# Performance work log

Measured on AMD Instinct MI355X. Metric: run time of the kernel, lower is better.

## Reference

```python
import jax, jax.numpy as jnp
import numpy as np

H = 512   # embedding_dim (forced by Attention(512,512))
F = 21    # n_features
T = 28    # output_length

def _cell(x, h, c, Wih, Whh, b):
    # PyTorch LSTMCell math, gate order i,f,g,o
    g = x @ Wih.T + h @ Whh.T + b
    i, f, gg, o = jnp.split(g, 4, axis=-1)
    c2 = jax.nn.sigmoid(f) * c + jax.nn.sigmoid(i) * jnp.tanh(gg)
    h2 = jax.nn.sigmoid(o) * jnp.tanh(c2)
    return h2, c2

def _lstm3(inp, h, c, Wih0, Wih1, Wih2, Whh, bih, bhh):
    # 3-layer LSTM, single time step. h,c: [3,1,H]
    Wihs = (Wih0, Wih1, Wih2)
    hs, cs = [], []
    x = inp
    for l in range(3):
        hl, cl = _cell(x, h[l], c[l], Wihs[l], Whh[l], bih[l] + bhh[l])
        hs.append(hl); cs.append(cl)
        x = hl
    return x, jnp.stack(hs), jnp.stack(cs)

def setup_inputs() -> dict:
    key = jax.random.key(0)
    ks = jax.random.split(key, 20)
    s = 0.05
    f32 = jnp.float32
    return {
        "x": jax.random.normal(ks[0], (1, F), f32),
        "prev_y": jax.random.normal(ks[1], (1, F), f32),
        "enc_Wih0": jax.random.normal(ks[2], (4*H, F), f32) * s,
        "enc_Wih1": jax.random.normal(ks[3], (4*H, H), f32) * s,
        "enc_Wih2": jax.random.normal(ks[4], (4*H, H), f32) * s,
        "enc_Whh": jax.random.normal(ks[5], (3, 4*H, H), f32) * s,
        "enc_bih": jax.random.normal(ks[6], (3, 4*H), f32) * s,
        "enc_bhh": jax.random.normal(ks[7], (3, 4*H), f32) * s,
        "attn_W": jax.random.normal(ks[8], (H, 2*H), f32) * s,
        "attn_b": jax.random.normal(ks[9], (H,), f32) * s,
        "v_W": jax.random.normal(ks[10], (1, H), f32) * s,
        "dec_Wih0": jax.random.normal(ks[11], (4*H, H+F), f32) * s,
        "dec_Wih1": jax.random.normal(ks[12], (4*H, H), f32) * s,
        "dec_Wih2": jax.random.normal(ks[13], (4*H, H), f32) * s,
        "dec_Whh": jax.random.normal(ks[14], (3, 4*H, H), f32) * s,
        "dec_bih": jax.random.normal(ks[15], (3, 4*H), f32) * s,
        "dec_bhh": jax.random.normal(ks[16], (3, 4*H), f32) * s,
        "out_W": jax.random.normal(ks[17], (F, 2*H), f32) * s,
        "out_b": jax.random.normal(ks[18], (F,), f32) * s,
    }

def reference(x, prev_y, enc_Wih0, enc_Wih1, enc_Wih2, enc_Whh, enc_bih, enc_bhh,
              attn_W, attn_b, v_W, dec_Wih0, dec_Wih1, dec_Wih2, dec_Whh, dec_bih, dec_bhh,
              out_W, out_b):
    z = jnp.zeros((3, 1, H), x.dtype)
    # Encoder: single time step over feature-as-sequence input [1, F]
    enc_out, h, c = _lstm3(x, z, z, enc_Wih0, enc_Wih1, enc_Wih2, enc_Whh, enc_bih, enc_bhh)
    # enc_out: [1, H]; src_len == 1

    def step(carry, _):
        prev_out, h, c = carry
        # Bahdanau attention (src_len = 1)
        cat = jnp.concatenate([h[2], enc_out], axis=-1)          # [1, 2H]
        energy = jnp.tanh(cat @ attn_W.T + attn_b)               # [1, H]
        score = energy @ v_W.T                                    # [1, 1]
        a = jax.nn.softmax(score, axis=1)                         # [1, 1] (== 1)
        weighted = a * enc_out                                    # [1, H]
        rnn_in = jnp.concatenate([prev_out, weighted], axis=-1)  # [1, H+F]
        out, h2, c2 = _lstm3(rnn_in, h, c, dec_Wih0, dec_Wih1, dec_Wih2, dec_Whh, dec_bih, dec_bhh)
        y = jnp.concatenate([out, weighted], axis=-1) @ out_W.T + out_b  # [1, F]
        return (y, h2, c2), y

    _, ys = jax.lax.scan(step, (prev_y, h, c), None, length=T)
    return ys  # [T, 1, F]
```

## Files before the change

### kernel.cpp

```cpp
#include <hip/hip_runtime.h>
#include <cstddef>

constexpr int H  = 512;
constexpr int F  = 21;
constexpr int T  = 28;
constexpr int NB = 128;
constexpr int NT = 256;
constexpr int NW = NT / 64;

#define SCOPE_AGENT __HIP_MEMORY_SCOPE_AGENT

__device__ unsigned long long g_hp[2][3][H];
__device__ unsigned g_exit;

struct P {
  const float *x, *py, *eW0, *eW1, *eW2, *ebih, *ebhh;
  const float *dW0, *dW1, *dW2, *dWhh, *dbih, *dbhh, *outW, *outb;
  float* out;
};

__device__ __forceinline__ float sigm(float v)  { return 1.0f / (1.0f + __expf(-v)); }
__device__ __forceinline__ float tanh_f(float v){ return 1.0f - 2.0f / (__expf(2.0f * v) + 1.0f); }

__device__ __forceinline__ float4 wredsum4(float4 v) {
#pragma unroll
  for (int off = 32; off > 0; off >>= 1) {
    v.x += __shfl_xor(v.x, off, 64);
    v.y += __shfl_xor(v.y, off, 64);
    v.z += __shfl_xor(v.z, off, 64);
    v.w += __shfl_xor(v.w, off, 64);
  }
  return v;
}
__device__ __forceinline__ float wredsum1(float v) {
#pragma unroll
  for (int off = 32; off > 0; off >>= 1) v += __shfl_xor(v, off, 64);
  return v;
}

__device__ __forceinline__ void pput(unsigned long long* slot, float v, unsigned tag) {
  union { float f; unsigned u; } c; c.f = v;
  unsigned long long pk = ((unsigned long long)tag << 32) | (unsigned long long)c.u;
  (void)__hip_atomic_exchange(slot, pk, __ATOMIC_RELAXED, SCOPE_AGENT);
}
__device__ __forceinline__ unsigned long long tld(const unsigned long long* q) {
  return __hip_atomic_load(q, __ATOMIC_RELAXED, SCOPE_AGENT);
}
__device__ __forceinline__ float fbits(unsigned long long v) {
  union { unsigned u; float f; } c; c.u = (unsigned)v; return c.f;
}

__device__ __forceinline__ void stagev(const unsigned long long* __restrict__ A,
                                       unsigned wa, float* __restrict__ dst) {
  const int i = threadIdx.x;
  unsigned long long v0 = tld(A + i), v1 = tld(A + i + NT);
  int guard = 0;
  while ((((unsigned)(v0 >> 32)) != wa || ((unsigned)(v1 >> 32)) != wa) &&
         ++guard < (1 << 20)) {
    v0 = tld(A + i); v1 = tld(A + i + NT);
  }
  dst[i] = fbits(v0); dst[i + NT] = fbits(v1);
  __syncthreads();
}

__device__ __forceinline__ void pollvec8(const unsigned long long* __restrict__ A,
                                         int lane, unsigned want, float4& x0, float4& x1) {
  const unsigned long long* q = A + lane * 8;
  unsigned long long v[8];
#pragma unroll
  for (int k = 0; k < 8; ++k) v[k] = tld(q + k);
  int guard = 0;
  for (;;) {
    bool ok = true;
#pragma unroll
    for (int k = 0; k < 8; ++k) ok &= ((unsigned)(v[k] >> 32) == want);
    if (ok || ++guard > (1 << 20)) break;
#pragma unroll
    for (int k = 0; k < 8; ++k) v[k] = tld(q + k);
  }
  x0 = make_float4(fbits(v[0]), fbits(v[1]), fbits(v[2]), fbits(v[3]));
  x1 = make_float4(fbits(v[4]), fbits(v[5]), fbits(v[6]), fbits(v[7]));
}

struct W8 { float4 a[4]; float4 b[4]; };

__device__ __forceinline__ W8 ldw_g(const float* __restrict__ W, int r, int lane) {
  W8 o;
#pragma unroll
  for (int g = 0; g < 4; ++g) {
    const float* q = W + (size_t)(g * H + r) * H + lane * 8;
    o.a[g] = *(const float4*)q;
    o.b[g] = *(const float4*)(q + 4);
  }
  return o;
}
__device__ __forceinline__ W8 ldw_lds(const float* sM, int w, int lane) {
  W8 o;
#pragma unroll
  for (int g = 0; g < 4; ++g) {
    const float* q = sM + (w * 4 + g) * H + lane * 8;
    o.a[g] = *(const float4*)q;
    o.b[g] = *(const float4*)(q + 4);
  }
  return o;
}
__device__ __forceinline__ void fma8(const W8& wt, const float4& x0, const float4& x1,
                                     float s[4]) {
#pragma unroll
  for (int g = 0; g < 4; ++g) {
    s[g] += wt.a[g].x * x0.x + wt.a[g].y * x0.y + wt.a[g].z * x0.z + wt.a[g].w * x0.w
          + wt.b[g].x * x1.x + wt.b[g].y * x1.y + wt.b[g].z * x1.z + wt.b[g].w * x1.w;
  }
}

__device__ __forceinline__ float cellup(const float4& v, const float b[4], float& c) {
  float cn = sigm(v.y + b[1]) * c + sigm(v.x + b[0]) * tanh_f(v.z + b[2]);
  c = cn;
  return sigm(v.w + b[3]) * tanh_f(cn);
}

__device__ __forceinline__ void write_y(const P& p, int trow, int w, int lane,
                                        const float4& h0, const float4& h1,
                                        const float* sYe) {
  for (int j = w; j < F; j += NW) {
    const float* q = p.outW + (size_t)j * (2 * H) + lane * 8;
    float4 w0 = *(const float4*)q;
    float4 w1 = *(const float4*)(q + 4);
    float s = w0.x * h0.x + w0.y * h0.y + w0.z * h0.z + w0.w * h0.w
            + w1.x * h1.x + w1.y * h1.y + w1.z * h1.z + w1.w * h1.w;
    s = wredsum1(s);
    if (lane == 0) p.out[trow * F + j] = s + sYe[j];
  }
}

__global__ __launch_bounds__(NT, 1)
void k_flow(P p) {
  const int lane = threadIdx.x & 63;
  const int w    = threadIdx.x >> 6;
  const int r    = blockIdx.x * NW + w;

  __shared__ float sM[NW * 4 * H];
  __shared__ float sBuf[2][H];
  __shared__ float senc[H];
  __shared__ float sYe[F + 3];
  __shared__ int   s_last;

  float c0 = 0.f, c1 = 0.f, c2 = 0.f;
  float b00[4], b0p[4], b1s[4], b2s[4];
  float sOld0[4] = {0, 0, 0, 0}, sOld1[4] = {0, 0, 0, 0}, sOld2[4] = {0, 0, 0, 0};
  int bi = 0;

  {
    float s0 = 0.f, s1 = 0.f, s2 = 0.f, s3 = 0.f;
    if (lane < F) {
      const float xv = p.x[lane];
      s0 = p.eW0[(size_t)(0 * H + r) * F + lane] * xv;
      s1 = p.eW0[(size_t)(1 * H + r) * F + lane] * xv;
      s2 = p.eW0[(size_t)(2 * H + r) * F + lane] * xv;
      s3 = p.eW0[(size_t)(3 * H + r) * F + lane] * xv;
    }
    float4 v = wredsum4(make_float4(s0, s1, s2, s3));
    if (lane == 0) {
      const float* bi_ = p.ebih + r;
      const float* bh_ = p.ebhh + r;
      float cn = sigm(v.x + bi_[0] + bh_[0]) * tanh_f(v.z + bi_[2 * H] + bh_[2 * H]);
      c0 = cn;
      pput(&g_hp[1][0][r], sigm(v.w + bi_[3 * H] + bh_[3 * H]) * tanh_f(cn), 1u);
    }
  }

  {
    float4 mA[4], mB[4];
#pragma unroll
    for (int g = 0; g < 4; ++g) {
      mA[g] = make_float4(0.f, 0.f, 0.f, 0.f);
      mB[g] = make_float4(0.f, 0.f, 0.f, 0.f);
    }
    for (int f = 0; f < F; ++f) {
      const float* q = p.outW + (size_t)f * (2 * H) + lane * 8;
      const float4 oa = *(const float4*)q;
      const float4 ob = *(const float4*)(q + 4);
#pragma unroll
      for (int g = 0; g < 4; ++g) {
        const float wf = p.dW0[(size_t)(g * H + r) * (H + F) + f];
        mA[g].x += wf * oa.x; mA[g].y += wf * oa.y; mA[g].z += wf * oa.z; mA[g].w += wf * oa.w;
        mB[g].x += wf * ob.x; mB[g].y += wf * ob.y; mB[g].z += wf * ob.z; mB[g].w += wf * ob.w;
      }
    }
#pragma unroll
    for (int g = 0; g < 4; ++g) {
      *(float4*)(sM + (w * 4 + g) * H + lane * 8)     = mA[g];
      *(float4*)(sM + (w * 4 + g) * H + lane * 8 + 4) = mB[g];
    }
  }
#pragma unroll
  for (int g = 0; g < 4; ++g) {
    b1s[g] = p.dbih[4 * H + g * H + r] + p.dbhh[4 * H + g * H + r];
    b2s[g] = p.dbih[8 * H + g * H + r] + p.dbhh[8 * H + g * H + r];
  }

  {
    W8 wt = ldw_g(p.eW1, r, lane);
    stagev(g_hp[1][0], 1u, sBuf[0]);
    float4 a0 = *(const float4*)(sBuf[0] + lane * 8);
    float4 a1 = *(const float4*)(sBuf[0] + lane * 8 + 4);
    float s[4] = {0.f, 0.f, 0.f, 0.f};
    fma8(wt, a0, a1, s);
    float4 v = wredsum4(make_float4(s[0], s[1], s[2], s[3]));
    if (lane == 0) {
      const float* bi_ = p.ebih + 4 * H + r;
      const float* bh_ = p.ebhh + 4 * H + r;
      float cn = sigm(v.x + bi_[0] + bh_[0]) * tanh_f(v.z + bi_[2 * H] + bh_[2 * H]);
      c1 = cn;
      pput(&g_hp[1][1][r], sigm(v.w + bi_[3 * H] + bh_[3 * H]) * tanh_f(cn), 1u);
    }
  }

  {
    W8 wt  = ldw_g(p.eW2, r, lane);
    W8 wh1 = ldw_g(p.dWhh + (size_t)4 * H * H, r, lane);
    stagev(g_hp[1][1], 1u, sBuf[1]);
    float4 a0 = *(const float4*)(sBuf[1] + lane * 8);
    float4 a1 = *(const float4*)(sBuf[1] + lane * 8 + 4);
    float s[4] = {0.f, 0.f, 0.f, 0.f};
    fma8(wt, a0, a1, s);
    float4 v = wredsum4(make_float4(s[0], s[1], s[2], s[3]));
    if (lane == 0) {
      const float* bi_ = p.ebih + 8 * H + r;
      const float* bh_ = p.ebhh + 8 * H + r;
      float cn = sigm(v.x + bi_[0] + bh_[0]) * tanh_f(v.z + bi_[2 * H] + bh_[2 * H]);
      c2 = cn;
      pput(&g_hp[1][2][r], sigm(v.w + bi_[3 * H] + bh_[3 * H]) * tanh_f(cn), 1u);
    }
    fma8(wh1, a0, a1, sOld1);
  }

  {
    W8 wh2 = ldw_g(p.dWhh + (size_t)8 * H * H, r, lane);
    stagev(g_hp[1][2], 1u, senc);
    float4 e0 = *(const float4*)(senc + lane * 8);
    float4 e1 = *(const float4*)(senc + lane * 8 + 4);
    for (int j = w; j < F; j += NW) {
      const float* q = p.outW + (size_t)j * (2 * H) + H + lane * 8;
      float4 w0 = *(const float4*)q;
      float4 w1 = *(const float4*)(q + 4);
      float s = w0.x * e0.x + w0.y * e0.y + w0.z * e0.z + w0.w * e0.w
              + w1.x * e1.x + w1.y * e1.y + w1.z * e1.z + w1.w * e1.w;
      s = wredsum1(s);
      if (lane == 0) sYe[j] = s + p.outb[j];
    }
    {
      float sg[4];
#pragma unroll
      for (int g = 0; g < 4; ++g) {
        const float* q = p.dW0 + (size_t)(g * H + r) * (H + F) + F + lane * 8;
        sg[g] = q[0] * e0.x + q[1] * e0.y + q[2] * e0.z + q[3] * e0.w
              + q[4] * e1.x + q[5] * e1.y + q[6] * e1.z + q[7] * e1.w;
      }
      float4 v = wredsum4(make_float4(sg[0], sg[1], sg[2], sg[3]));
      if (lane == 0) {
        b0p[0] = v.x + p.dbih[0 * H + r] + p.dbhh[0 * H + r];
        b0p[1] = v.y + p.dbih[1 * H + r] + p.dbhh[1 * H + r];
        b0p[2] = v.z + p.dbih[2 * H + r] + p.dbhh[2 * H + r];
        b0p[3] = v.w + p.dbih[3 * H + r] + p.dbhh[3 * H + r];
      }
    }
    {
      float f0 = 0.f, f1 = 0.f, f2 = 0.f, f3 = 0.f;
      if (lane < F) {
        const float yv = p.py[lane];
        f0 = p.dW0[(size_t)(0 * H + r) * (H + F) + lane] * yv;
        f1 = p.dW0[(size_t)(1 * H + r) * (H + F) + lane] * yv;
        f2 = p.dW0[(size_t)(2 * H + r) * (H + F) + lane] * yv;
        f3 = p.dW0[(size_t)(3 * H + r) * (H + F) + lane] * yv;
      }
      float4 v = wredsum4(make_float4(f0, f1, f2, f3));
      if (lane == 0) {
        b00[0] = b0p[0] + v.x; b00[1] = b0p[1] + v.y;
        b00[2] = b0p[2] + v.z; b00[3] = b0p[3] + v.w;
      }
    }
    __syncthreads();
    {
      float f0 = 0.f, f1 = 0.f, f2 = 0.f, f3 = 0.f;
      if (lane < F) {
        const float yv = sYe[lane];
        f0 = p.dW0[(size_t)(0 * H + r) * (H + F) + lane] * yv;
        f1 = p.dW0[(size_t)(1 * H + r) * (H + F) + lane] * yv;
        f2 = p.dW0[(size_t)(2 * H + r) * (H + F) + lane] * yv;
        f3 = p.dW0[(size_t)(3 * H + r) * (H + F) + lane] * yv;
      }
      float4 v = wredsum4(make_float4(f0, f1, f2, f3));
      if (lane == 0) {
        b0p[0] += v.x; b0p[1] += v.y; b0p[2] += v.z; b0p[3] += v.w;
      }
    }
    fma8(wh2, e0, e1, sOld2);
  }

  {
    W8 wh0 = ldw_g(p.dWhh, r, lane);
    float4 a0 = *(const float4*)(sBuf[0] + lane * 8);
    float4 a1 = *(const float4*)(sBuf[0] + lane * 8 + 4);
    float s[4] = {0.f, 0.f, 0.f, 0.f};
    fma8(wh0, a0, a1, s);
    float4 v = wredsum4(make_float4(s[0], s[1], s[2], s[3]));
    if (lane == 0) pput(&g_hp[0][0][r], cellup(v, b00, c0), 2u);
  }
  __syncthreads();

  for (int t = 0; t < T; ++t) {
    const int pb = t & 1, ob = pb ^ 1;
    const unsigned wn = (unsigned)(t + 2);
    const unsigned wo = (unsigned)(t + 1);

    if (t >= 1) {
      W8 wh2 = ldw_g(p.dWhh + (size_t)8 * H * H, r, lane);
      stagev(g_hp[ob][2], wo, sBuf[bi]);
      W8 wm = ldw_lds(sM, w, lane);
      float4 h20 = *(const float4*)(sBuf[bi] + lane * 8);
      float4 h21 = *(const float4*)(sBuf[bi] + lane * 8 + 4);
      float s[4] = {sOld0[0], sOld0[1], sOld0[2], sOld0[3]};
      fma8(wm, h20, h21, s);
      float4 v = wredsum4(make_float4(s[0], s[1], s[2], s[3]));
      if (lane == 0) pput(&g_hp[pb][0][r], cellup(v, b0p, c0), wn);
      if (blockIdx.x == (unsigned)t) write_y(p, t - 1, w, lane, h20, h21, sYe);
      sOld2[0] = sOld2[1] = sOld2[2] = sOld2[3] = 0.f;
      fma8(wh2, h20, h21, sOld2);
      bi ^= 1;
    }

    {
      W8 wi  = ldw_g(p.dW1, r, lane);
      W8 wh0 = ldw_g(p.dWhh, r, lane);
      stagev(g_hp[pb][0], wn, sBuf[bi]);
      float4 a0 = *(const float4*)(sBuf[bi] + lane * 8);
      float4 a1 = *(const float4*)(sBuf[bi] + lane * 8 + 4);
      float s[4] = {sOld1[0], sOld1[1], sOld1[2], sOld1[3]};
      fma8(wi, a0, a1, s);
      float4 v = wredsum4(make_float4(s[0], s[1], s[2], s[3]));
      if (lane == 0) pput(&g_hp[pb][1][r], cellup(v, b1s, c1), wn);
      sOld0[0] = sOld0[1] = sOld0[2] = sOld0[3] = 0.f;
      fma8(wh0, a0, a1, sOld0);
      bi ^= 1;
    }
    {
      W8 wi  = ldw_g(p.dW2, r, lane);
      W8 wh1 = ldw_g(p.dWhh + (size_t)4 * H * H, r, lane);
      stagev(g_hp[pb][1], wn, sBuf[bi]);
      float4 a0 = *(const float4*)(sBuf[bi] + lane * 8);
      float4 a1 = *(const float4*)(sBuf[bi] + lane * 8 + 4);
      float s[4] = {sOld2[0], sOld2[1], sOld2[2], sOld2[3]};
      fma8(wi, a0, a1, s);
      float4 v = wredsum4(make_float4(s[0], s[1], s[2], s[3]));
      if (lane == 0) pput(&g_hp[pb][2][r], cellup(v, b2s, c2), wn);
      sOld1[0] = sOld1[1] = sOld1[2] = sOld1[3] = 0.f;
      fma8(wh1, a0, a1, sOld1);
      bi ^= 1;
    }
  }

  if (blockIdx.x == (unsigned)T) {
    float4 h20, h21;
    pollvec8(g_hp[(T - 1) & 1][2], lane, (unsigned)(T + 1), h20, h21);
    write_y(p, T - 1, w, lane, h20, h21, sYe);
  }

  __syncthreads();
  if (threadIdx.x == 0) {
    unsigned old = __hip_atomic_fetch_add(&g_exit, 1u, __ATOMIC_RELAXED, SCOPE_AGENT);
    s_last = (old == NB - 1) ? 1 : 0;
  }
  __syncthreads();
  if (s_last) {
    unsigned long long* z = &g_hp[0][0][0];
    for (int i = threadIdx.x; i < 2 * 3 * H; i += NT)
      __hip_atomic_store(z + i, 0ull, __ATOMIC_RELAXED, SCOPE_AGENT);
    if (threadIdx.x == 0)
      __hip_atomic_store(&g_exit, 0u, __ATOMIC_RELAXED, SCOPE_AGENT);
  }
}

extern "C" void kernel_launch(void* const* d_in, const int* in_sizes, int n_in,
                              void* d_out, int out_size, void* d_ws, size_t ws_size,
                              hipStream_t stream) {
  P p;
  p.x    = (const float*)d_in[0];
  p.py   = (const float*)d_in[1];
  p.eW0  = (const float*)d_in[2];
  p.eW1  = (const float*)d_in[3];
  p.eW2  = (const float*)d_in[4];
  p.ebih = (const float*)d_in[6];
  p.ebhh = (const float*)d_in[7];
  p.dW0  = (const float*)d_in[11];
  p.dW1  = (const float*)d_in[12];
  p.dW2  = (const float*)d_in[13];
  p.dWhh = (const float*)d_in[14];
  p.dbih = (const float*)d_in[15];
  p.dbhh = (const float*)d_in[16];
  p.outW = (const float*)d_in[17];
  p.outb = (const float*)d_in[18];
  p.out  = (float*)d_out;

  hipLaunchKernelGGL(k_flow, dim3(NB), dim3(NT), 0, stream, p);
}
```

Measured before the change: 356.5 us.

## Move output projection to a dedicated extra block fed by per-step h buffers

Adds a 129th block that only computes the per-step output projection y, reading each step's top-layer hidden state from a new per-timestep global buffer g_hy. The recurrent blocks no longer run write_y on their critical path, and the final-step polling block is removed. In exchange, each step's top-layer store doubles, another block is launched, and there are more global buffers to clear at exit.

```diff
diff --git a/kernel.cpp b/kernel.cpp
--- a/kernel.cpp
+++ b/kernel.cpp
@@ -4,13 +4,15 @@
 constexpr int H  = 512;
 constexpr int F  = 21;
 constexpr int T  = 28;
-constexpr int NB = 128;
+constexpr int PB = 128;
+constexpr int NB = PB + 1;
 constexpr int NT = 256;
 constexpr int NW = NT / 64;
 
 #define SCOPE_AGENT __HIP_MEMORY_SCOPE_AGENT
 
 __device__ unsigned long long g_hp[2][3][H];
+__device__ unsigned long long g_hy[T][H];
 __device__ unsigned g_exit;
 
 struct P {
@@ -63,25 +65,6 @@
   __syncthreads();
 }
 
-__device__ __forceinline__ void pollvec8(const unsigned long long* __restrict__ A,
-                                         int lane, unsigned want, float4& x0, float4& x1) {
-  const unsigned long long* q = A + lane * 8;
-  unsigned long long v[8];
-#pragma unroll
-  for (int k = 0; k < 8; ++k) v[k] = tld(q + k);
-  int guard = 0;
-  for (;;) {
-    bool ok = true;
-#pragma unroll
-    for (int k = 0; k < 8; ++k) ok &= ((unsigned)(v[k] >> 32) == want);
-    if (ok || ++guard > (1 << 20)) break;
-#pragma unroll
-    for (int k = 0; k < 8; ++k) v[k] = tld(q + k);
-  }
-  x0 = make_float4(fbits(v[0]), fbits(v[1]), fbits(v[2]), fbits(v[3]));
-  x1 = make_float4(fbits(v[4]), fbits(v[5]), fbits(v[6]), fbits(v[7]));
-}
-
 struct W8 { float4 a[4]; float4 b[4]; };
 
 __device__ __forceinline__ W8 ldw_g(const float* __restrict__ W, int r, int lane) {
@@ -119,9 +102,9 @@
   return sigm(v.w + b[3]) * tanh_f(cn);
 }
 
-__device__ __forceinline__ void write_y(const P& p, int trow, int w, int lane,
-                                        const float4& h0, const float4& h1,
-                                        const float* sYe) {
+__device__ __forceinline__ void write_y_frag(const P& p, int trow, int w, int lane,
+                                             const float4& h0, const float4& h1,
+                                             const float* sYe) {
   for (int j = w; j < F; j += NW) {
     const float* q = p.outW + (size_t)j * (2 * H) + lane * 8;
     float4 w0 = *(const float4*)q;
@@ -137,7 +120,6 @@
 void k_flow(P p) {
   const int lane = threadIdx.x & 63;
   const int w    = threadIdx.x >> 6;
-  const int r    = blockIdx.x * NW + w;
 
   __shared__ float sM[NW * 4 * H];
   __shared__ float sBuf[2][H];
@@ -145,225 +127,249 @@
   __shared__ float sYe[F + 3];
   __shared__ int   s_last;
 
-  float c0 = 0.f, c1 = 0.f, c2 = 0.f;
-  float b00[4], b0p[4], b1s[4], b2s[4];
-  float sOld0[4] = {0, 0, 0, 0}, sOld1[4] = {0, 0, 0, 0}, sOld2[4] = {0, 0, 0, 0};
-  int bi = 0;
-
-  {
-    float s0 = 0.f, s1 = 0.f, s2 = 0.f, s3 = 0.f;
-    if (lane < F) {
-      const float xv = p.x[lane];
-      s0 = p.eW0[(size_t)(0 * H + r) * F + lane] * xv;
-      s1 = p.eW0[(size_t)(1 * H + r) * F + lane] * xv;
-      s2 = p.eW0[(size_t)(2 * H + r) * F + lane] * xv;
-      s3 = p.eW0[(size_t)(3 * H + r) * F + lane] * xv;
-    }
-    float4 v = wredsum4(make_float4(s0, s1, s2, s3));
-    if (lane == 0) {
-      const float* bi_ = p.ebih + r;
-      const float* bh_ = p.ebhh + r;
-      float cn = sigm(v.x + bi_[0] + bh_[0]) * tanh_f(v.z + bi_[2 * H] + bh_[2 * H]);
-      c0 = cn;
-      pput(&g_hp[1][0][r], sigm(v.w + bi_[3 * H] + bh_[3 * H]) * tanh_f(cn), 1u);
-    }
-  }
-
-  {
-    float4 mA[4], mB[4];
+  if (blockIdx.x == PB) {
+    stagev(g_hp[1][2], 1u, senc);
+    {
+      float4 e0 = *(const float4*)(senc + lane * 8);
+      float4 e1 = *(const float4*)(senc + lane * 8 + 4);
+      for (int j = w; j < F; j += NW) {
+        const float* q = p.outW + (size_t)j * (2 * H) + H + lane * 8;
+        float4 w0 = *(const float4*)q;
+        float4 w1 = *(const float4*)(q + 4);
+        float s = w0.x * e0.x + w0.y * e0.y + w0.z * e0.z + w0.w * e0.w
+                + w1.x * e1.x + w1.y * e1.y + w1.z * e1.z + w1.w * e1.w;
+        s = wredsum1(s);
+        if (lane == 0) sYe[j] = s + p.outb[j];
+      }
+      __syncthreads();
+    }
+    for (int t = 0; t < T; ++t) {
+      float* xb = sBuf[t & 1];
+      stagev(g_hy[t], (unsigned)(t + 2), xb);
+      float4 h20 = *(const float4*)(xb + lane * 8);
+      float4 h21 = *(const float4*)(xb + lane * 8 + 4);
+      write_y_frag(p, t, w, lane, h20, h21, sYe);
+    }
+  } else {
+    const int r = blockIdx.x * NW + w;
+
+    float c0 = 0.f, c1 = 0.f, c2 = 0.f;
+    float b00[4], b0p[4], b1s[4], b2s[4];
+    float sOld0[4] = {0, 0, 0, 0}, sOld1[4] = {0, 0, 0, 0}, sOld2[4] = {0, 0, 0, 0};
+    int bi = 0;
+
+    {
+      float s0 = 0.f, s1 = 0.f, s2 = 0.f, s3 = 0.f;
+      if (lane < F) {
+        const float xv = p.x[lane];
+        s0 = p.eW0[(size_t)(0 * H + r) * F + lane] * xv;
+        s1 = p.eW0[(size_t)(1 * H + r) * F + lane] * xv;
+        s2 = p.eW0[(size_t)(2 * H + r) * F + lane] * xv;
+        s3 = p.eW0[(size_t)(3 * H + r) * F + lane] * xv;
+      }
+      float4 v = wredsum4(make_float4(s0, s1, s2, s3));
+      if (lane == 0) {
+        const float* bi_ = p.ebih + r;
+        const float* bh_ = p.ebhh + r;
+        float cn = sigm(v.x + bi_[0] + bh_[0]) * tanh_f(v.z + bi_[2 * H] + bh_[2 * H]);
+        c0 = cn;
+        pput(&g_hp[1][0][r], sigm(v.w + bi_[3 * H] + bh_[3 * H]) * tanh_f(cn), 1u);
+      }
+    }
+
+    {
+      float4 mA[4], mB[4];
+#pragma unroll
+      for (int g = 0; g < 4; ++g) {
+        mA[g] = make_float4(0.f, 0.f, 0.f, 0.f);
+        mB[g] = make_float4(0.f, 0.f, 0.f, 0.f);
+      }
+      for (int f = 0; f < F; ++f) {
+        const float* q = p.outW + (size_t)f * (2 * H) + lane * 8;
+        const float4 oa = *(const float4*)q;
+        const float4 ob = *(const float4*)(q + 4);
+#pragma unroll
+        for (int g = 0; g < 4; ++g) {
+          const float wf = p.dW0[(size_t)(g * H + r) * (H + F) + f];
+          mA[g].x += wf * oa.x; mA[g].y += wf * oa.y; mA[g].z += wf * oa.z; mA[g].w += wf * oa.w;
+          mB[g].x += wf * ob.x; mB[g].y += wf * ob.y; mB[g].z += wf * ob.z; mB[g].w += wf * ob.w;
+        }
+      }
+#pragma unroll
+      for (int g = 0; g < 4; ++g) {
+        *(float4*)(sM + (w * 4 + g) * H + lane * 8)     = mA[g];
+        *(float4*)(sM + (w * 4 + g) * H + lane * 8 + 4) = mB[g];
+      }
+    }
 #pragma unroll
     for (int g = 0; g < 4; ++g) {
-      mA[g] = make_float4(0.f, 0.f, 0.f, 0.f);
-      mB[g] = make_float4(0.f, 0.f, 0.f, 0.f);
-    }
-    for (int f = 0; f < F; ++f) {
-      const float* q = p.outW + (size_t)f * (2 * H) + lane * 8;
-      const float4 oa = *(const float4*)q;
-      const float4 ob = *(const float4*)(q + 4);
-#pragma unroll
-      for (int g = 0; g < 4; ++g) {
-        const float wf = p.dW0[(size_t)(g * H + r) * (H + F) + f];
-        mA[g].x += wf * oa.x; mA[g].y += wf * oa.y; mA[g].z += wf * oa.z; mA[g].w += wf * oa.w;
-        mB[g].x += wf * ob.x; mB[g].y += wf * ob.y; mB[g].z += wf * ob.z; mB[g].w += wf * ob.w;
-      }
-    }
-#pragma unroll
-    for (int g = 0; g < 4; ++g) {
-      *(float4*)(sM + (w * 4 + g) * H + lane * 8)     = mA[g];
-      *(float4*)(sM + (w * 4 + g) * H + lane * 8 + 4) = mB[g];
-    }
-  }
-#pragma unroll
-  for (int g = 0; g < 4; ++g) {
-    b1s[g] = p.dbih[4 * H + g * H + r] + p.dbhh[4 * H + g * H + r];
-    b2s[g] = p.dbih[8 * H + g * H + r] + p.dbhh[8 * H + g * H + r];
-  }
-
-  {
-    W8 wt = ldw_g(p.eW1, r, lane);
-    stagev(g_hp[1][0], 1u, sBuf[0]);
-    float4 a0 = *(const float4*)(sBuf[0] + lane * 8);
-    float4 a1 = *(const float4*)(sBuf[0] + lane * 8 + 4);
-    float s[4] = {0.f, 0.f, 0.f, 0.f};
-    fma8(wt, a0, a1, s);
-    float4 v = wredsum4(make_float4(s[0], s[1], s[2], s[3]));
-    if (lane == 0) {
-      const float* bi_ = p.ebih + 4 * H + r;
-      const float* bh_ = p.ebhh + 4 * H + r;
-      float cn = sigm(v.x + bi_[0] + bh_[0]) * tanh_f(v.z + bi_[2 * H] + bh_[2 * H]);
-      c1 = cn;
-      pput(&g_hp[1][1][r], sigm(v.w + bi_[3 * H] + bh_[3 * H]) * tanh_f(cn), 1u);
-    }
-  }
-
-  {
-    W8 wt  = ldw_g(p.eW2, r, lane);
-    W8 wh1 = ldw_g(p.dWhh + (size_t)4 * H * H, r, lane);
-    stagev(g_hp[1][1], 1u, sBuf[1]);
-    float4 a0 = *(const float4*)(sBuf[1] + lane * 8);
-    float4 a1 = *(const float4*)(sBuf[1] + lane * 8 + 4);
-    float s[4] = {0.f, 0.f, 0.f, 0.f};
-    fma8(wt, a0, a1, s);
-    float4 v = wredsum4(make_float4(s[0], s[1], s[2], s[3]));
-    if (lane == 0) {
-      const float* bi_ = p.ebih + 8 * H + r;
-      const float* bh_ = p.ebhh + 8 * H + r;
-      float cn = sigm(v.x + bi_[0] + bh_[0]) * tanh_f(v.z + bi_[2 * H] + bh_[2 * H]);
-      c2 = cn;
-      pput(&g_hp[1][2][r], sigm(v.w + bi_[3 * H] + bh_[3 * H]) * tanh_f(cn), 1u);
-    }
-    fma8(wh1, a0, a1, sOld1);
-  }
-
-  {
-    W8 wh2 = ldw_g(p.dWhh + (size_t)8 * H * H, r, lane);
-    stagev(g_hp[1][2], 1u, senc);
-    float4 e0 = *(const float4*)(senc + lane * 8);
-    float4 e1 = *(const float4*)(senc + lane * 8 + 4);
-    for (int j = w; j < F; j += NW) {
-      const float* q = p.outW + (size_t)j * (2 * H) + H + lane * 8;
-      float4 w0 = *(const float4*)q;
-      float4 w1 = *(const float4*)(q + 4);
-      float s = w0.x * e0.x + w0.y * e0.y + w0.z * e0.z + w0.w * e0.w
-              + w1.x * e1.x + w1.y * e1.y + w1.z * e1.z + w1.w * e1.w;
-      s = wredsum1(s);
-      if (lane == 0) sYe[j] = s + p.outb[j];
-    }
-    {
-      float sg[4];
-#pragma unroll
-      for (int g = 0; g < 4; ++g) {
-        const float* q = p.dW0 + (size_t)(g * H + r) * (H + F) + F + lane * 8;
-        sg[g] = q[0] * e0.x + q[1] * e0.y + q[2] * e0.z + q[3] * e0.w
-              + q[4] * e1.x + q[5] * e1.y + q[6] * e1.z + q[7] * e1.w;
-      }
-      float4 v = wredsum4(make_float4(sg[0], sg[1], sg[2], sg[3]));
+      b1s[g] = p.dbih[4 * H + g * H + r] + p.dbhh[4 * H + g * H + r];
+      b2s[g] = p.dbih[8 * H + g * H + r] + p.dbhh[8 * H + g * H + r];
+    }
+
+    {
+      W8 wt = ldw_g(p.eW1, r, lane);
+      stagev(g_hp[1][0], 1u, sBuf[0]);
+      float4 a0 = *(const float4*)(sBuf[0] + lane * 8);
+      float4 a1 = *(const float4*)(sBuf[0] + lane * 8 + 4);
+      float s[4] = {0.f, 0.f, 0.f, 0.f};
+      fma8(wt, a0, a1, s);
+      float4 v = wredsum4(make_float4(s[0], s[1], s[2], s[3]));
       if (lane == 0) {
-        b0p[0] = v.x + p.dbih[0 * H + r] + p.dbhh[0 * H + r];
-        b0p[1] = v.y + p.dbih[1 * H + r] + p.dbhh[1 * H + r];
-        b0p[2] = v.z + p.dbih[2 * H + r] + p.dbhh[2 * H + r];
-        b0p[3] = v.w + p.dbih[3 * H + r] + p.dbhh[3 * H + r];
-      }
-    }
-    {
-      float f0 = 0.f, f1 = 0.f, f2 = 0.f, f3 = 0.f;
-      if (lane < F) {
-        const float yv = p.py[lane];
-        f0 = p.dW0[(size_t)(0 * H + r) * (H + F) + lane] * yv;
-        f1 = p.dW0[(size_t)(1 * H + r) * (H + F) + lane] * yv;
-        f2 = p.dW0[(size_t)(2 * H + r) * (H + F) + lane] * yv;
-        f3 = p.dW0[(size_t)(3 * H + r) * (H + F) + lane] * yv;
-      }
-      float4 v = wredsum4(make_float4(f0, f1, f2, f3));
+        const float* bi_ = p.ebih + 4 * H + r;
+        const float* bh_ = p.ebhh + 4 * H + r;
+        float cn = sigm(v.x + bi_[0] + bh_[0]) * tanh_f(v.z + bi_[2 * H] + bh_[2 * H]);
+        c1 = cn;
+        pput(&g_hp[1][1][r], sigm(v.w + bi_[3 * H] + bh_[3 * H]) * tanh_f(cn), 1u);
+      }
+    }
+
+    {
+      W8 wt  = ldw_g(p.eW2, r, lane);
+      W8 wh1 = ldw_g(p.dWhh + (size_t)4 * H * H, r, lane);
+      stagev(g_hp[1][1], 1u, sBuf[1]);
+      float4 a0 = *(const float4*)(sBuf[1] + lane * 8);
+      float4 a1 = *(const float4*)(sBuf[1] + lane * 8 + 4);
+      float s[4] = {0.f, 0.f, 0.f, 0.f};
+      fma8(wt, a0, a1, s);
+      float4 v = wredsum4(make_float4(s[0], s[1], s[2], s[3]));
       if (lane == 0) {
-        b00[0] = b0p[0] + v.x; b00[1] = b0p[1] + v.y;
-        b00[2] = b0p[2] + v.z; b00[3] = b0p[3] + v.w;
-      }
+        const float* bi_ = p.ebih + 8 * H + r;
+        const float* bh_ = p.ebhh + 8 * H + r;
+        float cn = sigm(v.x + bi_[0] + bh_[0]) * tanh_f(v.z + bi_[2 * H] + bh_[2 * H]);
+        c2 = cn;
+        pput(&g_hp[1][2][r], sigm(v.w + bi_[3 * H] + bh_[3 * H]) * tanh_f(cn), 1u);
+      }
+      fma8(wh1, a0, a1, sOld1);
+    }
+
+    {
+      W8 wh2 = ldw_g(p.dWhh + (size_t)8 * H * H, r, lane);
+      stagev(g_hp[1][2], 1u, senc);
+      float4 e0 = *(const float4*)(senc + lane * 8);
+      float4 e1 = *(const float4*)(senc + lane * 8 + 4);
+      for (int j = w; j < F; j += NW) {
+        const float* q = p.outW + (size_t)j * (2 * H) + H + lane * 8;
+        float4 w0 = *(const float4*)q;
+        float4 w1 = *(const float4*)(q + 4);
+        float s = w0.x * e0.x + w0.y * e0.y + w0.z * e0.z + w0.w * e0.w
+                + w1.x * e1.x + w1.y * e1.y + w1.z * e1.z + w1.w * e1.w;
+        s = wredsum1(s);
+        if (lane == 0) sYe[j] = s + p.outb[j];
+      }
+      {
+        float sg[4];
+#pragma unroll
+        for (int g = 0; g < 4; ++g) {
+          const float* q = p.dW0 + (size_t)(g * H + r) * (H + F) + F + lane * 8;
+          sg[g] = q[0] * e0.x + q[1] * e0.y + q[2] * e0.z + q[3] * e0.w
+                + q[4] * e1.x + q[5] * e1.y + q[6] * e1.z + q[7] * e1.w;
+        }
+        float4 v = wredsum4(make_float4(sg[0], sg[1], sg[2], sg[3]));
+        if (lane == 0) {
+          b0p[0] = v.x + p.dbih[0 * H + r] + p.dbhh[0 * H + r];
+          b0p[1] = v.y + p.dbih[1 * H + r] + p.dbhh[1 * H + r];
+          b0p[2] = v.z + p.dbih[2 * H + r] + p.dbhh[2 * H + r];
+          b0p[3] = v.w + p.dbih[3 * H + r] + p.dbhh[3 * H + r];
+        }
+      }
+      {
+        float f0 = 0.f, f1 = 0.f, f2 = 0.f, f3 = 0.f;
+        if (lane < F) {
+          const float yv = p.py[lane];
+          f0 = p.dW0[(size_t)(0 * H + r) * (H + F) + lane] * yv;
+          f1 = p.dW0[(size_t)(1 * H + r) * (H + F) + lane] * yv;
+          f2 = p.dW0[(size_t)(2 * H + r) * (H + F) + lane] * yv;
+          f3 = p.dW0[(size_t)(3 * H + r) * (H + F) + lane] * yv;
+        }
+        float4 v = wredsum4(make_float4(f0, f1, f2, f3));
+        if (lane == 0) {
+          b00[0] = b0p[0] + v.x; b00[1] = b0p[1] + v.y;
+          b00[2] = b0p[2] + v.z; b00[3] = b0p[3] + v.w;
+        }
+      }
+      __syncthreads();
+      {
+        float f0 = 0.f, f1 = 0.f, f2 = 0.f, f3 = 0.f;
+        if (lane < F) {
+          const float yv = sYe[lane];
+          f0 = p.dW0[(size_t)(0 * H + r) * (H + F) + lane] * yv;
+          f1 = p.dW0[(size_t)(1 * H + r) * (H + F) + lane] * yv;
+          f2 = p.dW0[(size_t)(2 * H + r) * (H + F) + lane] * yv;
+          f3 = p.dW0[(size_t)(3 * H + r) * (H + F) + lane] * yv;
+        }
+        float4 v = wredsum4(make_float4(f0, f1, f2, f3));
+        if (lane == 0) {
+          b0p[0] += v.x; b0p[1] += v.y; b0p[2] += v.z; b0p[3] += v.w;
+        }
+      }
+      fma8(wh2, e0, e1, sOld2);
+    }
+
+    {
+      W8 wh0 = ldw_g(p.dWhh, r, lane);
+      float4 a0 = *(const float4*)(sBuf[0] + lane * 8);
+      float4 a1 = *(const float4*)(sBuf[0] + lane * 8 + 4);
+      float s[4] = {0.f, 0.f, 0.f, 0.f};
+      fma8(wh0, a0, a1, s);
+      float4 v = wredsum4(make_float4(s[0], s[1], s[2], s[3]));
+      if (lane == 0) pput(&g_hp[0][0][r], cellup(v, b00, c0), 2u);
     }
     __syncthreads();
-    {
-      float f0 = 0.f, f1 = 0.f, f2 = 0.f, f3 = 0.f;
-      if (lane < F) {
-        const float yv = sYe[lane];
-        f0 = p.dW0[(size_t)(0 * H + r) * (H + F) + lane] * yv;
-        f1 = p.dW0[(size_t)(1 * H + r) * (H + F) + lane] * yv;
-        f2 = p.dW0[(size_t)(2 * H + r) * (H + F) + lane] * yv;
-        f3 = p.dW0[(size_t)(3 * H + r) * (H + F) + lane] * yv;
-      }
-      float4 v = wredsum4(make_float4(f0, f1, f2, f3));
-      if (lane == 0) {
-        b0p[0] += v.x; b0p[1] += v.y; b0p[2] += v.z; b0p[3] += v.w;
-      }
-    }
-    fma8(wh2, e0, e1, sOld2);
-  }
-
-  {
-    W8 wh0 = ldw_g(p.dWhh, r, lane);
-    float4 a0 = *(const float4*)(sBuf[0] + lane * 8);
-    float4 a1 = *(const float4*)(sBuf[0] + lane * 8 + 4);
-    float s[4] = {0.f, 0.f, 0.f, 0.f};
-    fma8(wh0, a0, a1, s);
-    float4 v = wredsum4(make_float4(s[0], s[1], s[2], s[3]));
-    if (lane == 0) pput(&g_hp[0][0][r], cellup(v, b00, c0), 2u);
-  }
-  __syncthreads();
-
-  for (int t = 0; t < T; ++t) {
-    const int pb = t & 1, ob = pb ^ 1;
-    const unsigned wn = (unsigned)(t + 2);
-    const unsigned wo = (unsigned)(t + 1);
-
-    if (t >= 1) {
-      W8 wh2 = ldw_g(p.dWhh + (size_t)8 * H * H, r, lane);
-      stagev(g_hp[ob][2], wo, sBuf[bi]);
-      W8 wm = ldw_lds(sM, w, lane);
-      float4 h20 = *(const float4*)(sBuf[bi] + lane * 8);
-      float4 h21 = *(const float4*)(sBuf[bi] + lane * 8 + 4);
-      float s[4] = {sOld0[0], sOld0[1], sOld0[2], sOld0[3]};
-      fma8(wm, h20, h21, s);
-      float4 v = wredsum4(make_float4(s[0], s[1], s[2], s[3]));
-      if (lane == 0) pput(&g_hp[pb][0][r], cellup(v, b0p, c0), wn);
-      if (blockIdx.x == (unsigned)t) write_y(p, t - 1, w, lane, h20, h21, sYe);
-      sOld2[0] = sOld2[1] = sOld2[2] = sOld2[3] = 0.f;
-      fma8(wh2, h20, h21, sOld2);
-      bi ^= 1;
-    }
-
-    {
-      W8 wi  = ldw_g(p.dW1, r, lane);
-      W8 wh0 = ldw_g(p.dWhh, r, lane);
-      stagev(g_hp[pb][0], wn, sBuf[bi]);
-      float4 a0 = *(const float4*)(sBuf[bi] + lane * 8);
-      float4 a1 = *(const float4*)(sBuf[bi] + lane * 8 + 4);
-      float s[4] = {sOld1[0], sOld1[1], sOld1[2], sOld1[3]};
-      fma8(wi, a0, a1, s);
-      float4 v = wredsum4(make_float4(s[0], s[1], s[2], s[3]));
-      if (lane == 0) pput(&g_hp[pb][1][r], cellup(v, b1s, c1), wn);
-      sOld0[0] = sOld0[1] = sOld0[2] = sOld0[3] = 0.f;
-      fma8(wh0, a0, a1, sOld0);
-      bi ^= 1;
-    }
-    {
-      W8 wi  = ldw_g(p.dW2, r, lane);
-      W8 wh1 = ldw_g(p.dWhh + (size_t)4 * H * H, r, lane);
-      stagev(g_hp[pb][1], wn, sBuf[bi]);
-      float4 a0 = *(const float4*)(sBuf[bi] + lane * 8);
-      float4 a1 = *(const float4*)(sBuf[bi] + lane * 8 + 4);
-      float s[4] = {sOld2[0], sOld2[1], sOld2[2], sOld2[3]};
-      fma8(wi, a0, a1, s);
-      float4 v = wredsum4(make_float4(s[0], s[1], s[2], s[3]));
-      if (lane == 0) pput(&g_hp[pb][2][r], cellup(v, b2s, c2), wn);
-      sOld1[0] = sOld1[1] = sOld1[2] = sOld1[3] = 0.f;
-      fma8(wh1, a0, a1, sOld1);
-      bi ^= 1;
-    }
-  }
-
-  if (blockIdx.x == (unsigned)T) {
-    float4 h20, h21;
-    pollvec8(g_hp[(T - 1) & 1][2], lane, (unsigned)(T + 1), h20, h21);
-    write_y(p, T - 1, w, lane, h20, h21, sYe);
+
+    for (int t = 0; t < T; ++t) {
+      const int pb = t & 1, ob = pb ^ 1;
+      const unsigned wn = (unsigned)(t + 2);
+      const unsigned wo = (unsigned)(t + 1);
+
+      if (t >= 1) {
+        W8 wh2 = ldw_g(p.dWhh + (size_t)8 * H * H, r, lane);
+        stagev(g_hp[ob][2], wo, sBuf[bi]);
+        W8 wm = ldw_lds(sM, w, lane);
+        float4 h20 = *(const float4*)(sBuf[bi] + lane * 8);
+        float4 h21 = *(const float4*)(sBuf[bi] + lane * 8 + 4);
+        float s[4] = {sOld0[0], sOld0[1], sOld0[2], sOld0[3]};
+        fma8(wm, h20, h21, s);
+        float4 v = wredsum4(make_float4(s[0], s[1], s[2], s[3]));
+        if (lane == 0) pput(&g_hp[pb][0][r], cellup(v, b0p, c0), wn);
+        sOld2[0] = sOld2[1] = sOld2[2] = sOld2[3] = 0.f;
+        fma8(wh2, h20, h21, sOld2);
+        bi ^= 1;
+      }
+
+      {
+        W8 wi  = ldw_g(p.dW1, r, lane);
+        W8 wh0 = ldw_g(p.dWhh, r, lane);
+        stagev(g_hp[pb][0], wn, sBuf[bi]);
+        float4 a0 = *(const float4*)(sBuf[bi] + lane * 8);
+        float4 a1 = *(const float4*)(sBuf[bi] + lane * 8 + 4);
+        float s[4] = {sOld1[0], sOld1[1], sOld1[2], sOld1[3]};
+        fma8(wi, a0, a1, s);
+        float4 v = wredsum4(make_float4(s[0], s[1], s[2], s[3]));
+        if (lane == 0) pput(&g_hp[pb][1][r], cellup(v, b1s, c1), wn);
+        sOld0[0] = sOld0[1] = sOld0[2] = sOld0[3] = 0.f;
+        fma8(wh0, a0, a1, sOld0);
+        bi ^= 1;
+      }
+      {
+        W8 wi  = ldw_g(p.dW2, r, lane);
+        W8 wh1 = ldw_g(p.dWhh + (size_t)4 * H * H, r, lane);
+        stagev(g_hp[pb][1], wn, sBuf[bi]);
+        float4 a0 = *(const float4*)(sBuf[bi] + lane * 8);
+        float4 a1 = *(const float4*)(sBuf[bi] + lane * 8 + 4);
+        float s[4] = {sOld2[0], sOld2[1], sOld2[2], sOld2[3]};
+        fma8(wi, a0, a1, s);
+        float4 v = wredsum4(make_float4(s[0], s[1], s[2], s[3]));
+        if (lane == 0) {
+          float hv = cellup(v, b2s, c2);
+          pput(&g_hp[pb][2][r], hv, wn);
+          pput(&g_hy[t][r], hv, wn);
+        }
+        sOld1[0] = sOld1[1] = sOld1[2] = sOld1[3] = 0.f;
+        fma8(wh1, a0, a1, sOld1);
+        bi ^= 1;
+      }
+    }
   }
 
   __syncthreads();
@@ -376,6 +382,9 @@
     unsigned long long* z = &g_hp[0][0][0];
     for (int i = threadIdx.x; i < 2 * 3 * H; i += NT)
       __hip_atomic_store(z + i, 0ull, __ATOMIC_RELAXED, SCOPE_AGENT);
+    unsigned long long* y = &g_hy[0][0];
+    for (int i = threadIdx.x; i < T * H; i += NT)
+      __hip_atomic_store(y + i, 0ull, __ATOMIC_RELAXED, SCOPE_AGENT);
     if (threadIdx.x == 0)
       __hip_atomic_store(&g_exit, 0u, __ATOMIC_RELAXED, SCOPE_AGENT);
   }
```

After: 317.9 us, median of 2. -10.8%, faster.
